# Kernel optimization log

Hardware: AMD Instinct MI355X
Metric: run time of the kernel (lower is better)

## Reference

```python
import jax, jax.numpy as jnp
import numpy as np
import math

B, L, C_IN = 256, 128, 75
D_EMB = 128      # DataEmbedding d_model
D_MODEL = 126    # encoder d_model (= L-2 after ODConv valid conv k=3)
H = 6
D_HEAD = D_MODEL // H  # 21
D_FF = 2048
FACTOR = 5
K_NUM = 4        # ODConv kernel_num (default)
ATT_CH = 16      # max(int(128*0.0625), 16)
EPS = 1e-5


def _ln(x, g, b):
    m = x.mean(-1, keepdims=True)
    v = ((x - m) ** 2).mean(-1, keepdims=True)
    return (x - m) * jax.lax.rsqrt(v + EPS) * g + b


def _bn_eval(x, g, b):
    # eval-mode BatchNorm, running_mean=0 running_var=1
    return x * (g / np.sqrt(1.0 + EPS)) + b


def _conv1d(x, w, b=None):
    out = jax.lax.conv_general_dilated(x, w, (1,), 'VALID',
                                       dimension_numbers=('NCH', 'OIH', 'NCH'))
    if b is not None:
        out = out + b[None, :, None]
    return out


def _pos_embed(n, d):
    pos = np.arange(n)[:, None].astype(np.float32)
    div = np.exp(np.arange(0, d, 2).astype(np.float32) * (-math.log(10000.0) / d))
    pe = np.zeros((n, d), np.float32)
    pe[:, 0::2] = np.sin(pos * div)
    pe[:, 1::2] = np.cos(pos * div)
    return jnp.asarray(pe)


def _prob_attention(Q, K, V, key):
    # Informer ProbAttention, mask_flag=False. Q,K,V: [B,H,Lq,D]
    b, h, lq, d = Q.shape
    lk = K.shape[2]
    u_keys = min(FACTOR * int(np.ceil(np.log(lk))), lk)
    n_top = min(FACTOR * int(np.ceil(np.log(lq))), lq)
    idx = jax.random.randint(key, (lq, u_keys), 0, lk)     # sampled key ids per query
    K_s = K[:, :, idx, :]                                  # [B,H,Lq,u,D]
    qks = jnp.einsum('bhld,bhlud->bhlu', Q, K_s)
    M = qks.max(-1) - qks.sum(-1) / lk                     # sparsity measure
    _, top = jax.lax.top_k(M, n_top)                       # [B,H,n_top]
    Qr = jnp.take_along_axis(Q, top[..., None], axis=2)    # [B,H,n_top,D]
    scores = jnp.einsum('bhud,bhkd->bhuk', Qr, K) / np.sqrt(d).astype(np.float32)
    upd = jnp.einsum('bhuk,bhkd->bhud', jax.nn.softmax(scores, -1), V)
    ctx = jnp.broadcast_to(V.mean(2, keepdims=True), Q.shape)  # initial context
    bi = jnp.arange(b)[:, None, None]
    hi = jnp.arange(h)[None, :, None]
    return ctx.at[bi, hi, top].set(upd)


def _forward(x_enc, x_mark_enc, token_w, time_w, time_b,
             od_fc_w, od_bn_g, od_bn_b, od_ch_w, od_ch_b, od_fil_w, od_fil_b,
             od_sp_w, od_sp_b, od_ker_w, od_ker_b, od_weight,
             q_w, q_b, k_w, k_b, v_w, v_b, o_w, o_b,
             ffn1_w, ffn1_b, ffn2_w, ffn2_b, ln1_g, ln1_b, ln2_g, ln2_b,
             cl_w, cl_b, cl_bn_g, cl_bn_b, enc_ln_g, enc_ln_b, fc_w, fc_b):
    # ---- DataEmbedding (token circular conv + pos + timeF linear; dropout=eval) ----
    xt = jnp.pad(x_enc.transpose(0, 2, 1), ((0, 0), (0, 0), (1, 1)), mode='wrap')
    tok = _conv1d(xt, token_w).transpose(0, 2, 1)          # [B,L,128]
    emb = tok + _pos_embed(L, D_EMB)[None] + (x_mark_enc @ time_w + time_b)

    # ---- ODConv1d(128,128,k=3,pad=0) on [B,128,L] ----
    x = emb.transpose(0, 2, 1)                             # [B,128,L]
    gap = x.mean(-1)                                       # [B,128]
    a = jax.nn.relu(_bn_eval(gap @ od_fc_w, od_bn_g, od_bn_b))   # [B,16]
    ch_att = jax.nn.sigmoid(a @ od_ch_w + od_ch_b)         # [B,128]
    fil_att = jax.nn.sigmoid(a @ od_fil_w + od_fil_b)      # [B,128]
    sp_att = jax.nn.sigmoid(a @ od_sp_w + od_sp_b)         # [B,3]
    ker_att = jax.nn.softmax(a @ od_ker_w + od_ker_b, -1)  # [B,4]
    xc = x * ch_att[:, :, None]
    agg_w = jnp.einsum('bn,bj,noij->boij', ker_att, sp_att, od_weight)  # [B,128,128,3]
    lout = L - 2
    patches = jnp.stack([xc[:, :, j:j + lout] for j in range(3)], axis=2)  # [B,128,3,126]
    x = jnp.einsum('boij,bijt->bot', agg_w, patches) * fil_att[:, :, None]  # [B,128,126]
    # encoder reads this as (seq=128, d_model=126)

    key = jax.random.key(42)

    def enc_layer(xx, i):
        b, l, _ = xx.shape
        Q = (xx @ q_w[i] + q_b[i]).reshape(b, l, H, D_HEAD).transpose(0, 2, 1, 3)
        Kk = (xx @ k_w[i] + k_b[i]).reshape(b, l, H, D_HEAD).transpose(0, 2, 1, 3)
        Vv = (xx @ v_w[i] + v_b[i]).reshape(b, l, H, D_HEAD).transpose(0, 2, 1, 3)
        ctx = _prob_attention(Q, Kk, Vv, jax.random.fold_in(key, i))
        new_x = ctx.transpose(0, 2, 1, 3).reshape(b, l, D_MODEL) @ o_w[i] + o_b[i]
        xx = _ln(xx + new_x, ln1_g[i], ln1_b[i])
        y = jax.nn.gelu(xx @ ffn1_w[i] + ffn1_b[i], approximate=False)
        y = y @ ffn2_w[i] + ffn2_b[i]
        return _ln(xx + y, ln2_g[i], ln2_b[i])

    x = enc_layer(x, 0)
    # ConvLayer distilling: circular conv k3 + BN + ELU + maxpool(k3,s2,p1): 128 -> 64
    xt = jnp.pad(x.transpose(0, 2, 1), ((0, 0), (0, 0), (1, 1)), mode='wrap')
    xt = _conv1d(xt, cl_w, cl_b)
    xt = jax.nn.elu(_bn_eval(xt, cl_bn_g[None, :, None], cl_bn_b[None, :, None]))
    xt = jax.lax.reduce_window(xt, -jnp.inf, jax.lax.max, (1, 1, 3), (1, 1, 2),
                               [(0, 0), (0, 0), (1, 1)])
    x = xt.transpose(0, 2, 1)                              # [B,64,126]
    x = enc_layer(x, 1)
    x = _ln(x, enc_ln_g, enc_ln_b)

    out = x.transpose(0, 2, 1) @ fc_w + fc_b               # [B,126,1]
    return out.transpose(0, 2, 1)                          # [B,1,126]


def setup_inputs() -> dict:
    key = jax.random.key(0)
    it = iter(jax.random.split(key, 48))
    def rn(shape, s=0.05):
        return jax.random.normal(next(it), shape, dtype=jnp.float32) * s
    return {
        'x_enc': jax.random.normal(next(it), (B, L, C_IN), jnp.float32),
        'x_mark_enc': jax.random.uniform(next(it), (B, L, 3), jnp.float32, -0.5, 0.5),
        'token_w': rn((D_EMB, C_IN, 3), 0.1),
        'time_w': rn((3, D_EMB), 0.1), 'time_b': rn((D_EMB,)),
        'od_fc_w': rn((D_EMB, ATT_CH), 0.1),
        'od_bn_g': jnp.ones((ATT_CH,)), 'od_bn_b': jnp.zeros((ATT_CH,)),
        'od_ch_w': rn((ATT_CH, D_EMB), 0.1), 'od_ch_b': rn((D_EMB,)),
        'od_fil_w': rn((ATT_CH, D_EMB), 0.1), 'od_fil_b': rn((D_EMB,)),
        'od_sp_w': rn((ATT_CH, 3), 0.1), 'od_sp_b': rn((3,)),
        'od_ker_w': rn((ATT_CH, K_NUM), 0.1), 'od_ker_b': rn((K_NUM,)),
        'od_weight': rn((K_NUM, D_EMB, D_EMB, 3), 0.05),
        'q_w': rn((2, D_MODEL, D_MODEL)), 'q_b': rn((2, D_MODEL)),
        'k_w': rn((2, D_MODEL, D_MODEL)), 'k_b': rn((2, D_MODEL)),
        'v_w': rn((2, D_MODEL, D_MODEL)), 'v_b': rn((2, D_MODEL)),
        'o_w': rn((2, D_MODEL, D_MODEL)), 'o_b': rn((2, D_MODEL)),
        'ffn1_w': rn((2, D_MODEL, D_FF), 0.03), 'ffn1_b': rn((2, D_FF)),
        'ffn2_w': rn((2, D_FF, D_MODEL), 0.03), 'ffn2_b': rn((2, D_MODEL)),
        'ln1_g': jnp.ones((2, D_MODEL)), 'ln1_b': jnp.zeros((2, D_MODEL)),
        'ln2_g': jnp.ones((2, D_MODEL)), 'ln2_b': jnp.zeros((2, D_MODEL)),
        'cl_w': rn((D_MODEL, D_MODEL, 3), 0.05), 'cl_b': rn((D_MODEL,)),
        'cl_bn_g': jnp.ones((D_MODEL,)), 'cl_bn_b': jnp.zeros((D_MODEL,)),
        'enc_ln_g': jnp.ones((D_MODEL,)), 'enc_ln_b': jnp.zeros((D_MODEL,)),
        'fc_w': rn((L // 2, 1), 0.1), 'fc_b': rn((1,)),
    }


def reference(x_enc, x_mark_enc, token_w, time_w, time_b,
              od_fc_w, od_bn_g, od_bn_b, od_ch_w, od_ch_b, od_fil_w, od_fil_b,
              od_sp_w, od_sp_b, od_ker_w, od_ker_b, od_weight,
              q_w, q_b, k_w, k_b, v_w, v_b, o_w, o_b,
              ffn1_w, ffn1_b, ffn2_w, ffn2_b, ln1_g, ln1_b, ln2_g, ln2_b,
              cl_w, cl_b, cl_bn_g, cl_bn_b, enc_ln_g, enc_ln_b, fc_w, fc_b):
    return _forward(x_enc, x_mark_enc, token_w, time_w, time_b,
                    od_fc_w, od_bn_g, od_bn_b, od_ch_w, od_ch_b, od_fil_w, od_fil_b,
                    od_sp_w, od_sp_b, od_ker_w, od_ker_b, od_weight,
                    q_w, q_b, k_w, k_b, v_w, v_b, o_w, o_b,
                    ffn1_w, ffn1_b, ffn2_w, ffn2_b, ln1_g, ln1_b, ln2_g, ln2_b,
                    cl_w, cl_b, cl_bn_g, cl_bn_b, enc_ln_g, enc_ln_b, fc_w, fc_b)
```

## Files before the change

kernel.cpp:

```cpp
#include <hip/hip_runtime.h>
#include <math.h>

#define NB 256
#define DM 126
#define DE 128
#define NH 6
#define DHd 21
#define DFF 2048
#define CIN 75
#define L0 128
#define NTOP 25

#ifndef IDX_MODE
#define IDX_MODE 0
#endif

typedef const float* fp;
typedef unsigned short u16;
typedef short s8v __attribute__((ext_vector_type(8)));
typedef float f4v __attribute__((ext_vector_type(4)));

__device__ __forceinline__ u16 f2bf(float x){
  unsigned u = __float_as_uint(x);
  unsigned r = (u + 0x7FFFu + ((u >> 16) & 1u)) >> 16;
  return (u16)r;
}
__device__ __forceinline__ float bf2f(u16 v){
  unsigned uu = ((unsigned)v) << 16;
  return __uint_as_float(uu);
}

__device__ __forceinline__ void gld_lds16(const u16* g, u16* l){
  __builtin_amdgcn_global_load_lds((const __attribute__((address_space(1))) unsigned int*)(const void*)g,
                                   (__attribute__((address_space(3))) unsigned int*)(void*)l,
                                   16, 0, 0);
}

__device__ __forceinline__ unsigned cvt_pk_bf16(float lo, float hi){
  unsigned r;
  asm("v_cvt_pk_bf16_f32 %0, %1, %2" : "=v"(r) : "v"(lo), "v"(hi));
  return r;
}

__device__ __forceinline__ void tf2(unsigned k0, unsigned k1, unsigned x0, unsigned x1,
                                    unsigned &o0, unsigned &o1){
  unsigned ks2 = k0 ^ k1 ^ 0x1BD11BDAu;
  x0 += k0; x1 += k1;
  #define RR(r) { x0 += x1; x1 = (x1 << (r)) | (x1 >> (32 - (r))); x1 ^= x0; }
  RR(13) RR(15) RR(26) RR(6)
  x0 += k1;  x1 += ks2 + 1u;
  RR(17) RR(29) RR(16) RR(24)
  x0 += ks2; x1 += k0 + 2u;
  RR(13) RR(15) RR(26) RR(6)
  x0 += k0;  x1 += k1 + 3u;
  RR(17) RR(29) RR(16) RR(24)
  x0 += k1;  x1 += ks2 + 4u;
  RR(13) RR(15) RR(26) RR(6)
  x0 += ks2; x1 += k0 + 5u;
  #undef RR
  o0 = x0; o1 = x1;
}

__global__ __launch_bounds__(256) void k_zero(float* out, int n){
  int i = blockIdx.x*256 + threadIdx.x;
  if (i < n) out[i] = 0.f;
}

__global__ __launch_bounds__(256) void k_idx(int* idx0, int* idx1){
  int tid = threadIdx.x;
  unsigned a0,a1,c0,c1;
  tf2(0u,42u, 0u,0u, a0,a1);
  tf2(0u,42u, 0u,1u, c0,c1);
  for (int f = tid; f < 3200; f += 256){
    unsigned y0,y1;
#if IDX_MODE==0
    tf2(a0,a1, 0u, (unsigned)(3200+f), y0,y1); idx0[f] = (int)(y1 & 127u);
#elif IDX_MODE==1
    tf2(a0,a1, 0u, (unsigned)(3200+f), y0,y1); idx0[f] = (int)(y0 & 127u);
#elif IDX_MODE==2
    tf2(a0,a1, (unsigned)f, (unsigned)(3200+f), y0,y1); idx0[f] = (int)(y1 & 127u);
#else
    tf2(a0,a1, (unsigned)f, (unsigned)(3200+f), y0,y1); idx0[f] = (int)(y0 & 127u);
#endif
  }
  for (int f = tid; f < 1600; f += 256){
    unsigned y0,y1;
#if IDX_MODE==0
    tf2(c0,c1, 0u, (unsigned)(1600+f), y0,y1); idx1[f] = (int)(y1 & 63u);
#elif IDX_MODE==1
    tf2(c0,c1, 0u, (unsigned)(1600+f), y0,y1); idx1[f] = (int)(y0 & 63u);
#elif IDX_MODE==2
    tf2(c0,c1, (unsigned)f, (unsigned)(1600+f), y0,y1); idx1[f] = (int)(y1 & 63u);
#else
    tf2(c0,c1, (unsigned)f, (unsigned)(1600+f), y0,y1); idx1[f] = (int)(y0 & 63u);
#endif
  }
}

__global__ __launch_bounds__(256) void k_wprep(fp token_w, fp clw,
                                               fp qw, fp qb, fp kw, fp kb, fp vw, fp vb, fp ow,
                                               fp f1w, fp f2w,
                                               u16* wemb, u16* wdist, u16* wqkv, u16* wo,
                                               u16* w1t, u16* w2t, float* qbias){
  int i = blockIdx.x*256 + threadIdx.x;
  if (i < 32768){
    int n = i >> 8, k = i & 255;
    float v = 0.f;
    if (k < 225){ int q = k/75, c = k - q*75; v = token_w[(size_t)n*225 + c*3 + q]; }
    wemb[i] = f2bf(v);
    return;
  }
  i -= 32768;
  if (i < 49152){
    int n = i / 384, k = i - n*384;
    float v = 0.f;
    if (n < DM && k < 378){ int q = k/126, ci = k - q*126; v = clw[((size_t)n*DM + ci)*3 + q]; }
    wdist[i] = f2bf(v);
    return;
  }
  i -= 49152;
  if (i < 2*49152){
    int layer = i / 49152, jj = i - layer*49152;
    int n = jj >> 7, k = jj & 127;
    int sec = n >> 7, nn = n & 127;
    const float* w = (sec == 0) ? qw : ((sec == 1) ? kw : vw);
    float v = (nn < DM && k < DM) ? w[((size_t)layer*DM + k)*DM + nn] : 0.f;
    wqkv[(size_t)layer*49152 + jj] = f2bf(v);
    return;
  }
  i -= 2*49152;
  if (i < 2*16384){
    int layer = i / 16384, jj = i - layer*16384;
    int n = jj >> 7, k = jj & 127;
    float v = (n < DM && k < DM) ? ow[(size_t)layer*DM*DM + k*DM + n] : 0.f;
    wo[(size_t)layer*16384 + jj] = f2bf(v);
    return;
  }
  i -= 2*16384;
  if (i < 2*262144){
    int layer = i / 262144, jj = i - layer*262144;
    int n = jj >> 7, k = jj & 127;
    float v = (k < DM) ? f1w[((size_t)layer*DM + k)*DFF + n] : 0.f;
    w1t[(size_t)layer*262144 + jj] = f2bf(v);
    return;
  }
  i -= 2*262144;
  if (i < 2*262144){
    int layer = i / 262144, jj = i - layer*262144;
    int n = jj >> 11, f = jj & 2047;
    float v = (n < DM) ? f2w[((size_t)layer*DFF + f)*DM + n] : 0.f;
    w2t[(size_t)layer*262144 + jj] = f2bf(v);
    return;
  }
  i -= 2*262144;
  if (i < 768){
    int layer = i / 384, n = i - layer*384;
    int sec = n >> 7, nn = n & 127;
    const float* bp = (sec == 0) ? qb : ((sec == 1) ? kb : vb);
    qbias[(size_t)layer*384 + n] = (nn < DM) ? bp[layer*DM + nn] : 0.f;
  }
}

__global__ __launch_bounds__(256) void k_front(fp x_enc, fp x_mark, const u16* wemb,
                                               fp time_w, fp time_b,
                                               fp fcw, fp bng, fp bnb,
                                               fp chw, fp chb, fp filw, fp filb,
                                               fp spw, fp spb, fp kerw, fp kerb,
                                               fp odw, float* xout){
  __shared__ __align__(16) u16 smem[71232];
  u16*   sXT = smem;
  u16*   sW  = smem + 17680;
  u16*   sA  = smem + 17680;
  float* sE  = reinterpret_cast<float*>(smem + 17680);
  float* red = reinterpret_cast<float*>(smem + 69904);
  float* gap = reinterpret_cast<float*>(smem + 70416);
  float* aAct= reinterpret_cast<float*>(smem + 70672);
  float* sch = reinterpret_cast<float*>(smem + 70704);
  float* sfil= reinterpret_cast<float*>(smem + 70960);
  float* ssp = reinterpret_cast<float*>(smem + 71216);
  float* sker= reinterpret_cast<float*>(smem + 71224);
  const int tid = threadIdx.x;
  const int wave = tid >> 6, lane = tid & 63, quad = lane >> 4, l15 = lane & 15;
  const int b = blockIdx.x;
  const f4v z4 = {0.f,0.f,0.f,0.f};
  const int mBase = wave * 32;

  {
    const float4* xb = reinterpret_cast<const float4*>(x_enc + (size_t)b*L0*CIN);
    for (int p4 = tid; p4 < (L0*CIN)/4; p4 += 256){
      float4 v4 = xb[p4];
      float vv[4] = {v4.x, v4.y, v4.z, v4.w};
      int e0 = p4*4;
      #pragma unroll
      for (int j = 0; j < 4; j++){
        int e = e0 + j;
        int sr = e / CIN, c = e - sr*CIN;
        u16 bv = f2bf(vv[j]);
        sA[((sr + 1) & 127)*264 + c] = bv;
        sA[sr*264 + 75 + c] = bv;
        sA[((sr + 127) & 127)*264 + 150 + c] = bv;
      }
    }
    for (int p = tid; p < 128*31; p += 256){
      int row = p / 31, c2 = p - row*31;
      sA[row*264 + 225 + c2] = 0;
    }
  }
  __syncthreads();
  {
    f4v acc[2][8];
    #pragma unroll
    for (int m = 0; m < 2; m++)
      #pragma unroll
      for (int t = 0; t < 8; t++) acc[m][t] = z4;
    for (int ks = 0; ks < 8; ks++){
      s8v a0 = *reinterpret_cast<const s8v*>(sA + (mBase + l15)*264 + ks*32 + quad*8);
      s8v a1 = *reinterpret_cast<const s8v*>(sA + (mBase + 16 + l15)*264 + ks*32 + quad*8);
      const u16* wb = wemb + (size_t)l15*256 + ks*32 + quad*8;
      #pragma unroll
      for (int t = 0; t < 8; t++){
        s8v bfr = *reinterpret_cast<const s8v*>(wb + (size_t)t*16*256);
        acc[0][t] = __builtin_amdgcn_mfma_f32_16x16x32_bf16(a0, bfr, acc[0][t], 0, 0, 0);
        acc[1][t] = __builtin_amdgcn_mfma_f32_16x16x32_bf16(a1, bfr, acc[1][t], 0, 0, 0);
      }
    }
    float divc[8], tw0c[8], tw1c[8], tw2c[8], tbc[8];
    #pragma unroll
    for (int t = 0; t < 8; t++){
      int col = t*16 + l15;
      int i2 = col >> 1;
      divc[t] = __expf((float)(2*i2) * (-9.210340371976184f / 128.f));
      tw0c[t] = time_w[col]; tw1c[t] = time_w[128 + col]; tw2c[t] = time_w[256 + col];
      tbc[t] = time_b[col];
    }
    #pragma unroll
    for (int m = 0; m < 2; m++){
      #pragma unroll
      for (int r = 0; r < 4; r++){
        int row = mBase + m*16 + quad*4 + r;
        const float* mk = x_mark + ((size_t)b*L0 + row)*3;
        float m0v = mk[0], m1v = mk[1], m2v = mk[2];
        #pragma unroll
        for (int t = 0; t < 8; t++){
          int col = t*16 + l15;
          float ang = (float)row * divc[t];
          float pe = (col & 1) ? __cosf(ang) : __sinf(ang);
          float tm = m0v*tw0c[t] + m1v*tw1c[t] + m2v*tw2c[t] + tbc[t];
          sE[row*132 + col] = acc[m][t][r] + pe + tm;
        }
      }
    }
  }
  __syncthreads();
  {
    int col = tid & 127, half = tid >> 7;
    float s = 0.f;
    for (int r = 0; r < 64; r++) s += sE[(half*64 + r)*132 + col];
    red[tid] = s;
  }
  __syncthreads();
  if (tid < 128) gap[tid] = (red[tid] + red[tid + 128]) * (1.f/128.f);
  __syncthreads();
  if (tid < 16){
    float acc = 0.f;
    for (int e = 0; e < DE; e++) acc += gap[e]*fcw[e*16 + tid];
    acc = acc * (bng[tid] / sqrtf(1.f + 1e-5f)) + bnb[tid];
    aAct[tid] = fmaxf(acc, 0.f);
  }
  __syncthreads();
  if (tid < 128){
    float accc = 0.f, accf = 0.f;
    for (int c = 0; c < 16; c++){ accc += aAct[c]*chw[c*DE + tid]; accf += aAct[c]*filw[c*DE + tid]; }
    sch[tid]  = 1.f/(1.f + __expf(-(accc + chb[tid])));
    sfil[tid] = 1.f/(1.f + __expf(-(accf + filb[tid])));
  } else if (tid < 131){
    int t = tid - 128;
    float acc = 0.f;
    for (int c = 0; c < 16; c++) acc += aAct[c]*spw[c*3 + t];
    ssp[t] = 1.f/(1.f + __expf(-(acc + spb[t])));
  } else if (tid == 132){
    float v[4]; float mx = -1e30f;
    for (int n = 0; n < 4; n++){
      float acc = 0.f;
      for (int c = 0; c < 16; c++) acc += aAct[c]*kerw[c*4 + n];
      v[n] = acc + kerb[n]; mx = fmaxf(mx, v[n]);
    }
    float ss = 0.f;
    for (int n = 0; n < 4; n++){ v[n] = __expf(v[n]-mx); ss += v[n]; }
    for (int n = 0; n < 4; n++) sker[n] = v[n]/ss;
  }
  __syncthreads();
  for (int p = tid; p < 130*128; p += 256){
    int l = p >> 7, i = p & 127;
    float v = (l < 128) ? sE[l*132 + i]*sch[i] : 0.f;
    sXT[l*136 + i] = f2bf(v);
  }
  __syncthreads();
  {
    float kr0 = sker[0], kr1 = sker[1], kr2 = sker[2], kr3 = sker[3];
    float spq[3]; spq[0] = ssp[0]; spq[1] = ssp[1]; spq[2] = ssp[2];
    const float4* od4 = (const float4*)odw;
    for (int p4 = tid; p4 < 128*384/4; p4 += 256){
      float4 w0 = od4[p4];
      float4 w1 = od4[12288 + p4];
      float4 w2 = od4[24576 + p4];
      float4 w3 = od4[36864 + p4];
      float vv[4] = { kr0*w0.x + kr1*w1.x + kr2*w2.x + kr3*w3.x,
                      kr0*w0.y + kr1*w1.y + kr2*w2.y + kr3*w3.y,
                      kr0*w0.z + kr1*w1.z + kr2*w2.z + kr3*w3.z,
                      kr0*w0.w + kr1*w1.w + kr2*w2.w + kr3*w3.w };
      int e0 = p4*4;
      #pragma unroll
      for (int j = 0; j < 4; j++){
        int e = e0 + j;
        int o = e / 384, rem = e - o*384;
        int i = rem / 3, q = rem - i*3;
        sW[(q*128 + o)*136 + i] = f2bf(vv[j] * spq[q]);
      }
    }
  }
  __syncthreads();
  {
    f4v acc[2][8];
    #pragma unroll
    for (int m = 0; m < 2; m++)
      #pragma unroll
      for (int t = 0; t < 8; t++) acc[m][t] = z4;
    for (int q = 0; q < 3; q++){
      const u16* wq = sW + q*128*136;
      #pragma unroll
      for (int ks = 0; ks < 4; ks++){
        s8v a0 = *reinterpret_cast<const s8v*>(wq + (mBase + l15)*136 + ks*32 + quad*8);
        s8v a1 = *reinterpret_cast<const s8v*>(wq + (mBase + 16 + l15)*136 + ks*32 + quad*8);
        #pragma unroll
        for (int t = 0; t < 8; t++){
          s8v bfr = *reinterpret_cast<const s8v*>(sXT + (t*16 + l15 + q)*136 + ks*32 + quad*8);
          acc[0][t] = __builtin_amdgcn_mfma_f32_16x16x32_bf16(a0, bfr, acc[0][t], 0, 0, 0);
          acc[1][t] = __builtin_amdgcn_mfma_f32_16x16x32_bf16(a1, bfr, acc[1][t], 0, 0, 0);
        }
      }
    }
    #pragma unroll
    for (int t = 0; t < 8; t++){
      int tt = t*16 + l15;
      if (tt < DM){
        #pragma unroll
        for (int m = 0; m < 2; m++){
          #pragma unroll
          for (int r = 0; r < 4; r++){
            int o = mBase + m*16 + quad*4 + r;
            xout[((size_t)b*DE + o)*DM + tt] = sfil[o] * acc[m][t][r];
          }
        }
      }
    }
  }
}

__global__ __launch_bounds__(256) void k_qkv_mfma(const float* xin, const u16* wqkv,
                                                  const float* qkvb, float* qkv,
                                                  float* vt, int L, int lshift, int lmask){
  __shared__ __align__(16) u16 sX[64*136];
  const int tid = threadIdx.x;
  const int wave = tid >> 6, lane = tid & 63, quad = lane >> 4, l15 = lane & 15;
  const size_t rows0 = (size_t)blockIdx.x * 64;
  for (int p = tid; p < 64*128; p += 256){
    int r = p >> 7, c = p & 127;
    float v = (c < DM) ? xin[(rows0 + r)*DM + c] : 0.f;
    sX[r*136 + c] = f2bf(v);
  }
  __syncthreads();
  const f4v z4 = {0.f,0.f,0.f,0.f};
  f4v acc[24];
  #pragma unroll
  for (int t = 0; t < 24; t++) acc[t] = z4;
  const int m0 = wave * 16;
  #pragma unroll
  for (int ks = 0; ks < 4; ks++){
    s8v a = *reinterpret_cast<const s8v*>(sX + (m0 + l15)*136 + ks*32 + quad*8);
    const u16* wb = wqkv + (size_t)l15*128 + ks*32 + quad*8;
    #pragma unroll
    for (int t = 0; t < 24; t++){
      s8v b = *reinterpret_cast<const s8v*>(wb + (size_t)t*16*128);
      acc[t] = __builtin_amdgcn_mfma_f32_16x16x32_bf16(a, b, acc[t], 0, 0, 0);
    }
  }
  #pragma unroll
  for (int t = 0; t < 24; t++){
    int col = t*16 + l15;
    float bv = qkvb[col];
    if (col < 256){
      #pragma unroll
      for (int r = 0; r < 4; r++){
        int row = m0 + quad*4 + r;
        qkv[(rows0 + row)*256 + col] = acc[t][r] + bv;
      }
    } else {
      int c = col - 256;
      if (c < DM){
        int h = c / DHd, d = c - h*DHd;
        #pragma unroll
        for (int r = 0; r < 4; r++){
          int gr = (int)rows0 + m0 + quad*4 + r;
          int b = gr >> lshift, l = gr & lmask;
          vt[((size_t)(b*NH + h)*DHd + d)*L + l] = acc[t][r] + bv;
        }
      }
    }
  }
}

__global__ __launch_bounds__(128) void k_attn(const float* qkv, const float* vt,
                                              const int* idx, int L,
                                              int* posmap, float* vmean, float* upd){
  __shared__ __align__(16) float sK[2816];
  __shared__ int sTop[32];
  const int tid = threadIdx.x;
  const int wave = tid >> 6, lane = tid & 63, quad = lane >> 4, l15 = lane & 15;
  const int bh = blockIdx.x;
  const int b = bh / NH, h = bh - b*NH;
  float* sM = sK + 2688;
  u16* sPb = reinterpret_cast<u16*>(sK);
  const float* qbase = qkv + (size_t)(b*L)*256 + h*DHd;
  const float* vb = vt + (size_t)bh*DHd*L;
  const f4v z4 = {0.f,0.f,0.f,0.f};
  const int ntn = L >> 4;
  const int d0 = quad*8;
  const int mt = wave;

  for (int p = tid; p < L*DHd; p += 128){
    int l = p / DHd, d = p - l*DHd;
    sK[p] = qbase[(size_t)l*256 + 128 + d];
  }
  posmap[bh*L0 + tid] = -1;
  __syncthreads();
  if (tid < L){
    const int l = tid;
    const float* qg = qbase + (size_t)l*256;
    float qr[DHd];
    #pragma unroll
    for (int d = 0; d < DHd; d++) qr[d] = qg[d];
    float mx = -1e30f, sm = 0.f;
    #pragma unroll
    for (int u = 0; u < NTOP; u++){
      int kk = idx[l*NTOP + u];
      const float* kp = sK + kk*DHd;
      float acc = 0.f;
      #pragma unroll
      for (int d = 0; d < DHd; d++) acc += qr[d]*kp[d];
      mx = fmaxf(mx, acc); sm += acc;
    }
    sM[l] = mx - sm/(float)L;
  }
  __syncthreads();
  if (wave == 0){
    for (int it = 0; it < NTOP; it++){
      float bv = sM[lane]; int bi = lane;
      if (L == 128){
        float v1 = sM[lane + 64];
        if (v1 > bv){ bv = v1; bi = lane + 64; }
      }
      #pragma unroll
      for (int off = 32; off > 0; off >>= 1){
        float ov = __shfl_xor(bv, off);
        int   oi = __shfl_xor(bi, off);
        if (ov > bv || (ov == bv && oi < bi)){ bv = ov; bi = oi; }
      }
      if (lane == 0){
        sM[bi] = -1e30f;
        posmap[bh*L0 + bi] = it;
        sTop[it] = bi;
      }
    }
  }
  __syncthreads();

  s8v aq;
  {
    int uu = mt*16 + l15; if (uu >= NTOP) uu = 0;
    int r = sTop[uu];
    const float* qp = qbase + (size_t)r*256 + d0;
    #pragma unroll
    for (int j = 0; j < 8; j++) aq[j] = (short)f2bf(qp[j]);
  }
  f4v sc[8];
  for (int nt = 0; nt < ntn; nt++){
    const float* kp = sK + (size_t)(nt*16 + l15)*DHd + d0;
    s8v bb;
    #pragma unroll
    for (int j = 0; j < 8; j++) bb[j] = (d0 + j < DHd) ? (short)f2bf(kp[j]) : (short)0;
    sc[nt] = __builtin_amdgcn_mfma_f32_16x16x32_bf16(aq, bb, z4, 0, 0, 0);
  }
  __syncthreads();
  const float inv21 = 0.21821789023599236f;
  #pragma unroll
  for (int r4 = 0; r4 < 4; r4++){
    float mx = -1e30f;
    for (int nt = 0; nt < ntn; nt++) mx = fmaxf(mx, sc[nt][r4]*inv21);
    #pragma unroll
    for (int off = 1; off < 16; off <<= 1) mx = fmaxf(mx, __shfl_xor(mx, off));
    float e[8]; float ss = 0.f;
    for (int nt = 0; nt < ntn; nt++){ e[nt] = __expf(sc[nt][r4]*inv21 - mx); ss += e[nt]; }
    #pragma unroll
    for (int off = 1; off < 16; off <<= 1) ss += __shfl_xor(ss, off);
    float dn = 1.f / ss;
    int u = mt*16 + quad*4 + r4;
    for (int nt = 0; nt < ntn; nt++)
      sPb[u*136 + nt*16 + l15] = f2bf(e[nt]*dn);
  }
  if (wave == 1){
    u16 invL = f2bf(1.f/(float)L);
    for (int c = lane; c < L; c += 64) sPb[25*136 + c] = invL;
  }
  f4v pv[2];
  pv[0] = z4; pv[1] = z4;
  int kSteps = L >> 5;
  for (int ks = 0; ks < kSteps; ks++){
    #pragma unroll
    for (int nt = 0; nt < 2; nt++){
      int d = nt*16 + l15;
      s8v bb;
      if (d < DHd){
        const float* vp = vb + (size_t)d*L + ks*32 + d0;
        #pragma unroll
        for (int j = 0; j < 8; j++) bb[j] = (short)f2bf(vp[j]);
      } else {
        #pragma unroll
        for (int j = 0; j < 8; j++) bb[j] = (short)0;
      }
      s8v a = *reinterpret_cast<const s8v*>(sPb + (mt*16 + l15)*136 + ks*32 + d0);
      pv[nt] = __builtin_amdgcn_mfma_f32_16x16x32_bf16(a, bb, pv[nt], 0, 0, 0);
    }
  }
  #pragma unroll
  for (int nt = 0; nt < 2; nt++){
    #pragma unroll
    for (int r4 = 0; r4 < 4; r4++){
      int u = mt*16 + quad*4 + r4;
      int d = nt*16 + l15;
      if (d < DHd){
        if (u < NTOP)       upd[((size_t)bh*NTOP + u)*DHd + d] = pv[nt][r4];
        else if (u == NTOP) vmean[bh*DHd + d] = pv[nt][r4];
      }
    }
  }
}

__global__ __launch_bounds__(256) void k_oproj_mfma(const float* xin, const float* vmean,
                                                    const int* posmap, const float* upd,
                                                    const u16* wo, fp ob, fp g, fp bb,
                                                    int layer, int lshift, int lmask, float* xmid){
  __shared__ __align__(16) float sOf[64*129];
  __shared__ float prs[128];
  __shared__ float smean[64], srstd[64];
  u16* sX = reinterpret_cast<u16*>(sOf);
  const int tid = threadIdx.x;
  const int wave = tid >> 6, lane = tid & 63, quad = lane >> 4, l15 = lane & 15;
  const int m0 = wave * 16;
  const size_t rows0 = (size_t)blockIdx.x * 64;
  for (int p = tid; p < 64*128; p += 256){
    int r = p >> 7, c = p & 127;
    int gr = (int)rows0 + r, b = gr >> lshift, l = gr & lmask;
    float v = 0.f;
    if (c < DM){
      int h = c / DHd, d = c - h*DHd;
      int bh = b*NH + h;
      int pos = posmap[bh*L0 + l];
      v = (pos >= 0) ? upd[((size_t)bh*NTOP + pos)*DHd + d] : vmean[bh*DHd + d];
    }
    sX[r*136 + c] = f2bf(v);
  }
  __syncthreads();
  const f4v z4 = {0.f,0.f,0.f,0.f};
  f4v acc[8];
  #pragma unroll
  for (int t = 0; t < 8; t++) acc[t] = z4;
  #pragma unroll
  for (int ks = 0; ks < 4; ks++){
    s8v a = *reinterpret_cast<const s8v*>(sX + (m0 + l15)*136 + ks*32 + quad*8);
    const u16* wb = wo + (size_t)l15*128 + ks*32 + quad*8;
    #pragma unroll
    for (int t = 0; t < 8; t++){
      s8v b = *reinterpret_cast<const s8v*>(wb + (size_t)t*16*128);
      acc[t] = __builtin_amdgcn_mfma_f32_16x16x32_bf16(a, b, acc[t], 0, 0, 0);
    }
  }
  __syncthreads();
  #pragma unroll
  for (int t = 0; t < 8; t++){
    int col = t*16 + l15;
    #pragma unroll
    for (int r = 0; r < 4; r++){
      sOf[(m0 + quad*4 + r)*129 + col] = acc[t][r];
    }
  }
  __syncthreads();
  const float* obl = ob + (size_t)layer*DM;
  for (int p = tid; p < 64*DM; p += 256){
    int r = p / DM, c = p - r*DM;
    sOf[r*129 + c] += xin[(rows0 + r)*DM + c] + obl[c];
  }
  __syncthreads();
  if (tid < 128){
    int row = tid >> 1, half = tid & 1;
    float s = 0.f;
    for (int c = half*63; c < half*63 + 63; c++) s += sOf[row*129 + c];
    prs[tid] = s;
  }
  __syncthreads();
  if (tid < 128 && (tid & 1) == 0) smean[tid>>1] = (prs[tid] + prs[tid+1]) / (float)DM;
  __syncthreads();
  if (tid < 128){
    int row = tid >> 1, half = tid & 1;
    float mn = smean[row];
    float s = 0.f;
    for (int c = half*63; c < half*63 + 63; c++){ float d = sOf[row*129 + c] - mn; s += d*d; }
    prs[tid] = s;
  }
  __syncthreads();
  if (tid < 128 && (tid & 1) == 0) srstd[tid>>1] = rsqrtf((prs[tid] + prs[tid+1])/(float)DM + 1e-5f);
  __syncthreads();
  const float* gl = g  + (size_t)layer*DM;
  const float* bl = bb + (size_t)layer*DM;
  for (int p = tid; p < 64*DM; p += 256){
    int r = p / DM, c = p - r*DM;
    xmid[(rows0 + r)*DM + c] = (sOf[r*129 + c] - smean[r])*srstd[r]*gl[c] + bl[c];
  }
}

__device__ __forceinline__ float gelu_fast(float x){
  float x2 = x*x;
  float u = x * __builtin_fmaf(0.10295128f, x2, 2.30212056f);
  u = fminf(u, 126.f);
#if __has_builtin(__builtin_amdgcn_exp2f)
  float t = __builtin_amdgcn_exp2f(u);
#else
  float t = __expf(u * 0.69314718056f);
#endif
  return x * t * __builtin_amdgcn_rcpf(t + 1.f);
}


__device__ __forceinline__ void stage_w1_p(const u16* w1t, int j, u16* buf, int p){
  int n = p >> 4, c = p & 15;
  int cg = c ^ (n & 7);
  gld_lds16(w1t + (((size_t)(j*64 + n)) << 7) + cg*8,
            buf + (size_t)((p >> 6) << 6)*8);
}
__device__ __forceinline__ void stage_w2_p(const u16* w2t, int j, u16* buf, int p){
  int n = p >> 3, c = p & 7;
  int cg = c ^ (n & 7);
  gld_lds16(w2t + (size_t)n*2048 + j*64 + cg*8,
            buf + (size_t)((p >> 6) << 6)*8);
}

__device__ __forceinline__ int yaddr(int row, int col){
  return row*64 + (((col >> 3) ^ (row & 7)) << 3) + (col & 7);
}

__device__ __forceinline__ void lgkm_barrier(){
  asm volatile("s_waitcnt lgkmcnt(0)" ::: "memory");
  __builtin_amdgcn_sched_barrier(0);
  __builtin_amdgcn_s_barrier();
  __builtin_amdgcn_sched_barrier(0);
}

template<int NT>
__global__ __launch_bounds__(NT) void k_ffn(const float* xmid, const u16* w1t, const u16* w2t,
                                            fp b1, fp b2w, fp g, fp bb, int layer, float* xout){
  constexpr int ROWS = NT/8;
  constexpr int NMG  = NT/256;
  constexpr int SYG  = NMG*2048;
  constexpr int SP   = 1024/NT;
  __shared__ __align__(16) u16 smem[SYG + 4*8192];
  __shared__ float prs[2*ROWS];
  __shared__ float smean[ROWS], srstd[ROWS];
  u16* wA0 = smem + SYG;
  u16* wA1 = wA0 + 8192;
  u16* wB0 = wA1 + 8192;
  u16* wB1 = wB0 + 8192;
  const int tid  = threadIdx.x;
  const int wave = tid >> 6, lane = tid & 63, quad = lane >> 4, l15 = lane & 15;
  const int mg = wave >> 2, ng = wave & 3;
  const int rowb = mg * 32;
  u16* sYg = smem + mg*2048;
  const size_t rows0 = (size_t)blockIdx.x * ROWS;

  s8v aX[2][4];
  #pragma unroll
  for (int mt = 0; mt < 2; mt++){
    const float* xr = xmid + (rows0 + rowb + mt*16 + l15)*(size_t)DM;
    #pragma unroll
    for (int ks = 0; ks < 4; ks++){
      #pragma unroll
      for (int j = 0; j < 8; j++){
        int c = ks*32 + quad*8 + j;
        float v = (c < DM) ? xr[c] : 0.f;
        aX[mt][ks][j] = (short)f2bf(v);
      }
    }
  }
  #pragma unroll
  for (int r = 0; r < SP; r++){
    stage_w1_p(w1t, 0, wA0, r*NT + tid);
    stage_w2_p(w2t, 0, wB0, r*NT + tid);
  }

  const float* b1l = b1 + (size_t)layer*DFF;
  const f4v z4 = {0.f, 0.f, 0.f, 0.f};
  f4v acc2[2][2];
  acc2[0][0]=z4; acc2[0][1]=z4; acc2[1][0]=z4; acc2[1][1]=z4;

  for (int j = 0; j < 32; j++){
    u16* wAcur = (j & 1) ? wA1 : wA0;
    u16* wAnxt = (j & 1) ? wA0 : wA1;
    u16* wBcur = (j & 1) ? wB1 : wB0;
    u16* wBnxt = (j & 1) ? wB0 : wB1;
    __syncthreads();
    if (j < 31){
      #pragma unroll
      for (int r = 0; r < SP; r++){
        stage_w1_p(w1t, j+1, wAnxt, r*NT + tid);
        stage_w2_p(w2t, j+1, wBnxt, r*NT + tid);
      }
    }
    f4v acc1[2];
    acc1[0] = z4; acc1[1] = z4;
    {
      int nloc = ng*16 + l15;
      #pragma unroll
      for (int ks = 0; ks < 4; ks++){
        int cg = (ks*4 + quad) ^ (nloc & 7);
        s8v b = *reinterpret_cast<const s8v*>(wAcur + nloc*128 + cg*8);
        acc1[0] = __builtin_amdgcn_mfma_f32_16x16x32_bf16(aX[0][ks], b, acc1[0], 0, 0, 0);
        acc1[1] = __builtin_amdgcn_mfma_f32_16x16x32_bf16(aX[1][ks], b, acc1[1], 0, 0, 0);
      }
    }
    {
      int col = ng*16 + l15;
      float bv = b1l[j*64 + col];
      #pragma unroll
      for (int mt = 0; mt < 2; mt++){
        float y0 = gelu_fast(acc1[mt][0] + bv);
        float y1 = gelu_fast(acc1[mt][1] + bv);
        float y2 = gelu_fast(acc1[mt][2] + bv);
        float y3 = gelu_fast(acc1[mt][3] + bv);
        unsigned p01 = cvt_pk_bf16(y0, y1);
        unsigned p23 = cvt_pk_bf16(y2, y3);
        int r0 = mt*16 + quad*4;
        sYg[yaddr(r0,     col)] = (u16)p01;
        sYg[yaddr(r0 + 1, col)] = (u16)(p01 >> 16);
        sYg[yaddr(r0 + 2, col)] = (u16)p23;
        sYg[yaddr(r0 + 3, col)] = (u16)(p23 >> 16);
      }
    }
    lgkm_barrier();
    #pragma unroll
    for (int ks2 = 0; ks2 < 2; ks2++){
      int ga = ((ks2*4 + quad) ^ (l15 & 7)) << 3;
      s8v a0 = *reinterpret_cast<const s8v*>(sYg + (l15)*64 + ga);
      s8v a1 = *reinterpret_cast<const s8v*>(sYg + (16 + l15)*64 + ga);
      #pragma unroll
      for (int t = 0; t < 2; t++){
        int nloc = ng*32 + t*16 + l15;
        int cg = (ks2*4 + quad) ^ (nloc & 7);
        s8v b = *reinterpret_cast<const s8v*>(wBcur + nloc*64 + cg*8);
        acc2[0][t] = __builtin_amdgcn_mfma_f32_16x16x32_bf16(a0, b, acc2[0][t], 0, 0, 0);
        acc2[1][t] = __builtin_amdgcn_mfma_f32_16x16x32_bf16(a1, b, acc2[1][t], 0, 0, 0);
      }
    }
  }

  __syncthreads();
  float* sO = reinterpret_cast<float*>(smem);
  #pragma unroll
  for (int mt = 0; mt < 2; mt++)
    #pragma unroll
    for (int t = 0; t < 2; t++)
      #pragma unroll
      for (int r = 0; r < 4; r++)
        sO[(rowb + mt*16 + quad*4 + r)*129 + ng*32 + t*16 + l15] = acc2[mt][t][r];
  __syncthreads();
  const float* b2l = b2w + (size_t)layer*DM;
  for (int p = tid; p < ROWS*DM; p += NT){
    int r = p / DM, c = p - r*DM;
    sO[r*129 + c] += b2l[c] + xmid[(rows0 + r)*DM + c];
  }
  __syncthreads();
  if (tid < 2*ROWS){
    int row = tid >> 1, half = tid & 1;
    float s = 0.f;
    for (int c = half*63; c < half*63 + 63; c++) s += sO[row*129 + c];
    prs[tid] = s;
  }
  __syncthreads();
  if (tid < 2*ROWS && (tid & 1) == 0) smean[tid>>1] = (prs[tid] + prs[tid+1]) / (float)DM;
  __syncthreads();
  if (tid < 2*ROWS){
    int row = tid >> 1, half = tid & 1;
    float mn = smean[row];
    float s = 0.f;
    for (int c = half*63; c < half*63 + 63; c++){ float d = sO[row*129 + c] - mn; s += d*d; }
    prs[tid] = s;
  }
  __syncthreads();
  if (tid < 2*ROWS && (tid & 1) == 0) srstd[tid>>1] = rsqrtf((prs[tid] + prs[tid+1])/(float)DM + 1e-5f);
  __syncthreads();
  const float* gl = g  + (size_t)layer*DM;
  const float* bl = bb + (size_t)layer*DM;
  for (int p = tid; p < ROWS*DM; p += NT){
    int r = p / DM, c = p - r*DM;
    xout[(rows0 + r)*DM + c] = (sO[r*129 + c] - smean[r])*srstd[r]*gl[c] + bl[c];
  }
}

__global__ __launch_bounds__(256) void k_distill_mfma(const float* xin, const u16* wdist,
                                                      fp clb, fp bng, fp bnb, float* xout){
  __shared__ __align__(16) u16 sA[128*392];
  const int tid = threadIdx.x;
  const int wave = tid >> 6, lane = tid & 63, quad = lane >> 4, l15 = lane & 15;
  const int b = blockIdx.x;
  for (int row = wave; row < 128; row += 4){
    #pragma unroll
    for (int e = 0; e < 6; e++){
      int kk = lane + e*64;
      float v = 0.f;
      if (kk < 378){
        int q = kk / 126, ci = kk - q*126;
        int sr = (row - 1 + q + 128) & 127;
        v = xin[((size_t)b*128 + sr)*DM + ci];
      }
      sA[row*392 + kk] = f2bf(v);
    }
  }
  __syncthreads();
  const f4v z4 = {0.f,0.f,0.f,0.f};
  f4v acc[2][8];
  #pragma unroll
  for (int m = 0; m < 2; m++)
    #pragma unroll
    for (int t = 0; t < 8; t++) acc[m][t] = z4;
  const int mBase = wave * 32;
  for (int ks = 0; ks < 12; ks++){
    s8v a0 = *reinterpret_cast<const s8v*>(sA + (mBase + l15)*392 + ks*32 + quad*8);
    s8v a1 = *reinterpret_cast<const s8v*>(sA + (mBase + 16 + l15)*392 + ks*32 + quad*8);
    const u16* wb = wdist + (size_t)l15*384 + ks*32 + quad*8;
    #pragma unroll
    for (int t = 0; t < 8; t++){
      s8v bfr = *reinterpret_cast<const s8v*>(wb + (size_t)t*16*384);
      acc[0][t] = __builtin_amdgcn_mfma_f32_16x16x32_bf16(a0, bfr, acc[0][t], 0, 0, 0);
      acc[1][t] = __builtin_amdgcn_mfma_f32_16x16x32_bf16(a1, bfr, acc[1][t], 0, 0, 0);
    }
  }
  __syncthreads();
  float* zsh = reinterpret_cast<float*>(sA);
  const float bnscale = 1.f / sqrtf(1.f + 1e-5f);
  #pragma unroll
  for (int t = 0; t < 8; t++){
    int co = t*16 + l15;
    if (co < DM){
      float cb = clb[co];
      float gg = bng[co] * bnscale, bv = bnb[co];
      #pragma unroll
      for (int m = 0; m < 2; m++){
        #pragma unroll
        for (int r = 0; r < 4; r++){
          int row = mBase + m*16 + quad*4 + r;
          float z = (acc[m][t][r] + cb)*gg + bv;
          z = (z > 0.f) ? z : (__expf(z) - 1.f);
          zsh[row*130 + co] = z;
        }
      }
    }
  }
  __syncthreads();
  for (int p = tid; p < 64*DM; p += 256){
    int j = p / DM, co = p - j*DM;
    float best = zsh[(2*j)*130 + co];
    if (j > 0) best = fmaxf(best, zsh[(2*j - 1)*130 + co]);
    best = fmaxf(best, zsh[(2*j + 1)*130 + co]);
    xout[((size_t)b*64 + j)*DM + co] = best;
  }
}

__global__ __launch_bounds__(128) void k_final(const float* xin, fp g, fp bb,
                                               fp fcw, fp fcb, float* out){
  __shared__ float xs[64][DM];
  __shared__ float mean_s[64], rstd_s[64];
  int b = blockIdx.x, t = threadIdx.x;
  for (int p = t; p < 64*DM; p += 128){ xs[p/DM][p%DM] = xin[(size_t)b*64*DM + p]; }
  __syncthreads();
  if (t < 64){
    float s = 0.f;
    for (int m = 0; m < DM; m++) s += xs[t][m];
    float mn = s / (float)DM;
    float v = 0.f;
    for (int m = 0; m < DM; m++){ float d = xs[t][m] - mn; v += d*d; }
    mean_s[t] = mn; rstd_s[t] = rsqrtf(v / (float)DM + 1e-5f);
  }
  __syncthreads();
  if (t < DM){
    float gv = g[t], bv = bb[t];
    float acc = fcb[0];
    for (int l = 0; l < 64; l++){
      float xn = (xs[l][t] - mean_s[l])*rstd_s[l]*gv + bv;
      acc += xn * fcw[l];
    }
    out[b*DM + t] = acc;
  }
}

extern "C" void kernel_launch(void* const* d_in, const int* in_sizes, int n_in,
                              void* d_out, int out_size, void* d_ws, size_t ws_size,
                              hipStream_t stream) {
  fp x_enc   = (fp)d_in[0];
  fp x_mark  = (fp)d_in[1];
  fp token_w = (fp)d_in[2];
  fp time_w  = (fp)d_in[3];
  fp time_b  = (fp)d_in[4];
  fp od_fc_w = (fp)d_in[5];
  fp od_bn_g = (fp)d_in[6];
  fp od_bn_b = (fp)d_in[7];
  fp od_ch_w = (fp)d_in[8];
  fp od_ch_b = (fp)d_in[9];
  fp od_fil_w= (fp)d_in[10];
  fp od_fil_b= (fp)d_in[11];
  fp od_sp_w = (fp)d_in[12];
  fp od_sp_b = (fp)d_in[13];
  fp od_ker_w= (fp)d_in[14];
  fp od_ker_b= (fp)d_in[15];
  fp od_wt   = (fp)d_in[16];
  fp q_w = (fp)d_in[17]; fp q_b = (fp)d_in[18];
  fp k_w = (fp)d_in[19]; fp k_b = (fp)d_in[20];
  fp v_w = (fp)d_in[21]; fp v_b = (fp)d_in[22];
  fp o_w = (fp)d_in[23]; fp o_b = (fp)d_in[24];
  fp f1w = (fp)d_in[25]; fp f1b = (fp)d_in[26];
  fp f2w = (fp)d_in[27]; fp f2b = (fp)d_in[28];
  fp ln1g= (fp)d_in[29]; fp ln1b= (fp)d_in[30];
  fp ln2g= (fp)d_in[31]; fp ln2b= (fp)d_in[32];
  fp cl_w= (fp)d_in[33]; fp cl_b= (fp)d_in[34];
  fp clbg= (fp)d_in[35]; fp clbb= (fp)d_in[36];
  fp elng= (fp)d_in[37]; fp elnb= (fp)d_in[38];
  fp fc_w= (fp)d_in[39]; fp fc_b= (fp)d_in[40];

  const size_t OFF_IDX0 = 0;
  const size_t OFF_IDX1 = OFF_IDX0 + 3200;
  const size_t OFF_CH   = OFF_IDX1 + 1600;
  const size_t OFF_FIL  = OFF_CH  + (size_t)NB*DE;
  const size_t OFF_SP   = OFF_FIL + (size_t)NB*DE;
  const size_t OFF_KER  = OFF_SP  + (size_t)NB*4;
  const size_t OFF_VM   = OFF_KER + (size_t)NB*4;
  const size_t OFF_POS  = OFF_VM  + (size_t)NB*NH*DHd;
  const size_t OFF_UPD  = OFF_POS + (size_t)NB*NH*L0;
  const size_t OFF_STOP = OFF_UPD + (size_t)NB*NH*NTOP*DHd;
  const size_t OFF_WTS  = (OFF_STOP + (size_t)NB*NH*NTOP + 255) & ~(size_t)255;
  const size_t WTS_FLOATS = (2*262144 + 2*262144 + 2*49152 + 2*16384 + 49152 + 32768)/2 + 2*384;
  const size_t OFF_BIG  = (OFF_WTS + WTS_FLOATS + 255) & ~(size_t)255;
  const size_t SBUF     = (size_t)NB*DE*L0;
  const size_t TOTAL    = OFF_BIG + 4*SBUF;

  if (ws_size < TOTAL*sizeof(float)){
    hipLaunchKernelGGL(k_zero, dim3((out_size+255)/256), dim3(256), 0, stream,
                       (float*)d_out, out_size);
    return;
  }

  float* ws = (float*)d_ws;
  int* idx0 = (int*)(ws + OFF_IDX0);
  int* idx1 = (int*)(ws + OFF_IDX1);
  float* vme = ws + OFF_VM;
  int* posm  = (int*)(ws + OFF_POS);
  float* updb= ws + OFF_UPD;
  u16* w1tb  = (u16*)(ws + OFF_WTS);
  u16* w2tb  = w1tb + 2*262144;
  u16* wqkvb = w2tb + 2*262144;
  u16* wob   = wqkvb + 2*49152;
  u16* wdistb= wob + 2*16384;
  u16* wembb = wdistb + 49152;
  float* qkvbias = (float*)(wembb + 32768);

  float* X    = ws + OFF_BIG;
  float* QKV  = X + SBUF;
  float* VT   = X + 3*SBUF;
  float* xmid = QKV;
  float* ffno = QKV + SBUF;

  hipLaunchKernelGGL(k_idx, dim3(1), dim3(256), 0, stream, idx0, idx1);
  hipLaunchKernelGGL(k_wprep, dim3(4931), dim3(256), 0, stream,
                     token_w, cl_w, q_w, q_b, k_w, k_b, v_w, v_b, o_w, f1w, f2w,
                     wembb, wdistb, wqkvb, wob, w1tb, w2tb, qkvbias);
  hipLaunchKernelGGL(k_front, dim3(NB), dim3(256), 0, stream,
                     x_enc, x_mark, wembb, time_w, time_b,
                     od_fc_w, od_bn_g, od_bn_b, od_ch_w, od_ch_b, od_fil_w, od_fil_b,
                     od_sp_w, od_sp_b, od_ker_w, od_ker_b, od_wt, X);

  hipLaunchKernelGGL(k_qkv_mfma, dim3(NB*L0/64), dim3(256), 0, stream,
                     X, wqkvb, qkvbias, QKV, VT, 128, 7, 127);
  hipLaunchKernelGGL(k_attn, dim3(NB*NH), dim3(128), 0, stream,
                     QKV, VT, idx0, L0, posm, vme, updb);
  hipLaunchKernelGGL(k_oproj_mfma, dim3(NB*L0/64), dim3(256), 0, stream,
                     X, vme, posm, updb, wob, o_b, ln1g, ln1b, 0, 7, 127, xmid);
  hipLaunchKernelGGL((k_ffn<1024>), dim3(NB*L0/128), dim3(1024), 0, stream,
                     xmid, w1tb, w2tb, f1b, f2b, ln2g, ln2b, 0, ffno);

  hipLaunchKernelGGL(k_distill_mfma, dim3(NB), dim3(256), 0, stream,
                     ffno, wdistb, cl_b, clbg, clbb, X);

  hipLaunchKernelGGL(k_qkv_mfma, dim3(NB*64/64), dim3(256), 0, stream,
                     X, wqkvb + 49152, qkvbias + 384, QKV, VT, 64, 6, 63);
  hipLaunchKernelGGL(k_attn, dim3(NB*NH), dim3(128), 0, stream,
                     QKV, VT, idx1, 64, posm, vme, updb);
  hipLaunchKernelGGL(k_oproj_mfma, dim3(NB*64/64), dim3(256), 0, stream,
                     X, vme, posm, updb, wob + 16384, o_b, ln1g, ln1b, 1, 6, 63, xmid);
  hipLaunchKernelGGL((k_ffn<512>), dim3(NB*64/64), dim3(512), 0, stream,
                     xmid, w1tb + 262144, w2tb + 262144, f1b, f2b, ln2g, ln2b, 1, ffno);

  hipLaunchKernelGGL(k_final, dim3(NB), dim3(128), 0, stream,
                     ffno, elng, elnb, fc_w, fc_b, (float*)d_out);
  (void)in_sizes; (void)n_in; (void)out_size; (void)ws_size;
}
```

Baseline: 613.9 us.

## Software-pipeline FFN GEMM1 and GEMM2 across iterations to drop mid-loop barrier

Restructures the fused FFN loop so GEMM2 for chunk j-1 runs in the same iteration as GEMM1+GELU for chunk j. The GELU output buffer is double-buffered and the W2 staging ring grows to four slots. This removes the second barrier per iteration and lets the two MFMA phases overlap. In exchange it uses more LDS per block, which may reduce occupancy, and it adds one extra loop iteration to drain the pipeline.

```diff
diff --git a/kernel.cpp b/kernel.cpp
--- a/kernel.cpp
+++ b/kernel.cpp
@@ -658,32 +658,23 @@
   return row*64 + (((col >> 3) ^ (row & 7)) << 3) + (col & 7);
 }
 
-__device__ __forceinline__ void lgkm_barrier(){
-  asm volatile("s_waitcnt lgkmcnt(0)" ::: "memory");
-  __builtin_amdgcn_sched_barrier(0);
-  __builtin_amdgcn_s_barrier();
-  __builtin_amdgcn_sched_barrier(0);
-}
-
 template<int NT>
 __global__ __launch_bounds__(NT) void k_ffn(const float* xmid, const u16* w1t, const u16* w2t,
                                             fp b1, fp b2w, fp g, fp bb, int layer, float* xout){
   constexpr int ROWS = NT/8;
   constexpr int NMG  = NT/256;
-  constexpr int SYG  = NMG*2048;
+  constexpr int SYG  = NMG*4096;
   constexpr int SP   = 1024/NT;
-  __shared__ __align__(16) u16 smem[SYG + 4*8192];
+  __shared__ __align__(16) u16 smem[SYG + 2*8192 + 4*8192];
   __shared__ float prs[2*ROWS];
   __shared__ float smean[ROWS], srstd[ROWS];
-  u16* wA0 = smem + SYG;
-  u16* wA1 = wA0 + 8192;
-  u16* wB0 = wA1 + 8192;
-  u16* wB1 = wB0 + 8192;
+  u16* wA = smem + SYG;
+  u16* wB = wA + 2*8192;
   const int tid  = threadIdx.x;
   const int wave = tid >> 6, lane = tid & 63, quad = lane >> 4, l15 = lane & 15;
   const int mg = wave >> 2, ng = wave & 3;
   const int rowb = mg * 32;
-  u16* sYg = smem + mg*2048;
+  u16* sYmg = smem + mg*4096;
   const size_t rows0 = (size_t)blockIdx.x * ROWS;
 
   s8v aX[2][4];
@@ -702,8 +693,9 @@
   }
   #pragma unroll
   for (int r = 0; r < SP; r++){
-    stage_w1_p(w1t, 0, wA0, r*NT + tid);
-    stage_w2_p(w2t, 0, wB0, r*NT + tid);
+    stage_w1_p(w1t, 0, wA, r*NT + tid);
+    stage_w2_p(w2t, 0, wB, r*NT + tid);
+    stage_w2_p(w2t, 1, wB + 8192, r*NT + tid);
   }
 
   const float* b1l = b1 + (size_t)layer*DFF;
@@ -711,62 +703,69 @@
   f4v acc2[2][2];
   acc2[0][0]=z4; acc2[0][1]=z4; acc2[1][0]=z4; acc2[1][1]=z4;
 
-  for (int j = 0; j < 32; j++){
-    u16* wAcur = (j & 1) ? wA1 : wA0;
-    u16* wAnxt = (j & 1) ? wA0 : wA1;
-    u16* wBcur = (j & 1) ? wB1 : wB0;
-    u16* wBnxt = (j & 1) ? wB0 : wB1;
+  for (int j = 0; j <= 32; j++){
     __syncthreads();
-    if (j < 31){
-      #pragma unroll
-      for (int r = 0; r < SP; r++){
-        stage_w1_p(w1t, j+1, wAnxt, r*NT + tid);
-        stage_w2_p(w2t, j+1, wBnxt, r*NT + tid);
-      }
-    }
-    f4v acc1[2];
-    acc1[0] = z4; acc1[1] = z4;
-    {
-      int nloc = ng*16 + l15;
-      #pragma unroll
-      for (int ks = 0; ks < 4; ks++){
-        int cg = (ks*4 + quad) ^ (nloc & 7);
-        s8v b = *reinterpret_cast<const s8v*>(wAcur + nloc*128 + cg*8);
-        acc1[0] = __builtin_amdgcn_mfma_f32_16x16x32_bf16(aX[0][ks], b, acc1[0], 0, 0, 0);
-        acc1[1] = __builtin_amdgcn_mfma_f32_16x16x32_bf16(aX[1][ks], b, acc1[1], 0, 0, 0);
-      }
-    }
-    {
-      int col = ng*16 + l15;
-      float bv = b1l[j*64 + col];
-      #pragma unroll
-      for (int mt = 0; mt < 2; mt++){
-        float y0 = gelu_fast(acc1[mt][0] + bv);
-        float y1 = gelu_fast(acc1[mt][1] + bv);
-        float y2 = gelu_fast(acc1[mt][2] + bv);
-        float y3 = gelu_fast(acc1[mt][3] + bv);
-        unsigned p01 = cvt_pk_bf16(y0, y1);
-        unsigned p23 = cvt_pk_bf16(y2, y3);
-        int r0 = mt*16 + quad*4;
-        sYg[yaddr(r0,     col)] = (u16)p01;
-        sYg[yaddr(r0 + 1, col)] = (u16)(p01 >> 16);
-        sYg[yaddr(r0 + 2, col)] = (u16)p23;
-        sYg[yaddr(r0 + 3, col)] = (u16)(p23 >> 16);
-      }
-    }
-    lgkm_barrier();
-    #pragma unroll
-    for (int ks2 = 0; ks2 < 2; ks2++){
-      int ga = ((ks2*4 + quad) ^ (l15 & 7)) << 3;
-      s8v a0 = *reinterpret_cast<const s8v*>(sYg + (l15)*64 + ga);
-      s8v a1 = *reinterpret_cast<const s8v*>(sYg + (16 + l15)*64 + ga);
-      #pragma unroll
-      for (int t = 0; t < 2; t++){
-        int nloc = ng*32 + t*16 + l15;
-        int cg = (ks2*4 + quad) ^ (nloc & 7);
-        s8v b = *reinterpret_cast<const s8v*>(wBcur + nloc*64 + cg*8);
-        acc2[0][t] = __builtin_amdgcn_mfma_f32_16x16x32_bf16(a0, b, acc2[0][t], 0, 0, 0);
-        acc2[1][t] = __builtin_amdgcn_mfma_f32_16x16x32_bf16(a1, b, acc2[1][t], 0, 0, 0);
+    if (j < 32){
+      if (j + 1 < 32){
+        #pragma unroll
+        for (int r = 0; r < SP; r++)
+          stage_w1_p(w1t, j+1, wA + ((j+1)&1)*8192, r*NT + tid);
+      }
+      if (j + 2 < 32){
+        #pragma unroll
+        for (int r = 0; r < SP; r++)
+          stage_w2_p(w2t, j+2, wB + ((j+2)&3)*8192, r*NT + tid);
+      }
+      u16* wAcur = wA + (j&1)*8192;
+      f4v acc1[2];
+      acc1[0] = z4; acc1[1] = z4;
+      {
+        int nloc = ng*16 + l15;
+        #pragma unroll
+        for (int ks = 0; ks < 4; ks++){
+          int cg = (ks*4 + quad) ^ (nloc & 7);
+          s8v b = *reinterpret_cast<const s8v*>(wAcur + nloc*128 + cg*8);
+          acc1[0] = __builtin_amdgcn_mfma_f32_16x16x32_bf16(aX[0][ks], b, acc1[0], 0, 0, 0);
+          acc1[1] = __builtin_amdgcn_mfma_f32_16x16x32_bf16(aX[1][ks], b, acc1[1], 0, 0, 0);
+        }
+      }
+      {
+        u16* sYw = sYmg + (j&1)*2048;
+        int col = ng*16 + l15;
+        float bv = b1l[j*64 + col];
+        #pragma unroll
+        for (int mt = 0; mt < 2; mt++){
+          float y0 = gelu_fast(acc1[mt][0] + bv);
+          float y1 = gelu_fast(acc1[mt][1] + bv);
+          float y2 = gelu_fast(acc1[mt][2] + bv);
+          float y3 = gelu_fast(acc1[mt][3] + bv);
+          unsigned p01 = cvt_pk_bf16(y0, y1);
+          unsigned p23 = cvt_pk_bf16(y2, y3);
+          int r0 = mt*16 + quad*4;
+          sYw[yaddr(r0,     col)] = (u16)p01;
+          sYw[yaddr(r0 + 1, col)] = (u16)(p01 >> 16);
+          sYw[yaddr(r0 + 2, col)] = (u16)p23;
+          sYw[yaddr(r0 + 3, col)] = (u16)(p23 >> 16);
+        }
+      }
+    }
+    if (j >= 1){
+      int jj = j - 1;
+      u16* sYr = sYmg + (jj&1)*2048;
+      u16* wBcur = wB + (jj&3)*8192;
+      #pragma unroll
+      for (int ks2 = 0; ks2 < 2; ks2++){
+        int ga = ((ks2*4 + quad) ^ (l15 & 7)) << 3;
+        s8v a0 = *reinterpret_cast<const s8v*>(sYr + (l15)*64 + ga);
+        s8v a1 = *reinterpret_cast<const s8v*>(sYr + (16 + l15)*64 + ga);
+        #pragma unroll
+        for (int t = 0; t < 2; t++){
+          int nloc = ng*32 + t*16 + l15;
+          int cg = (ks2*4 + quad) ^ (nloc & 7);
+          s8v b = *reinterpret_cast<const s8v*>(wBcur + nloc*64 + cg*8);
+          acc2[0][t] = __builtin_amdgcn_mfma_f32_16x16x32_bf16(a0, b, acc2[0][t], 0, 0, 0);
+          acc2[1][t] = __builtin_amdgcn_mfma_f32_16x16x32_bf16(a1, b, acc2[1][t], 0, 0, 0);
+        }
       }
     }
   }
```

Measured after the change: 617.3 us. No clear change (+0.5%).
